# Kernel tuning notes

Hardware: AMD Instinct MI355X
Metric: run time of the kernel (lower is better)

The kernel has to match this reference:

```python
import jax, jax.numpy as jnp
import numpy as np
from jax import lax

# --- constants from init_kwargs ---
B, N = 1, 6
C_IN, MID, C_CTX, D = 512, 512, 80, 112
OGH, OGW = 256, 704
DSF = 16
FH, FW = OGH // DSF, OGW // DSF  # 16, 44
D_MIN, D_MAX = 2.0, 58.0
NX, NY, NZ = 128, 128, 1
VOXEL_SIZE = np.array([0.8, 0.8, 8.0], np.float32)
VOXEL_COORD = np.array([-51.2 + 0.4, -51.2 + 0.4, -5.0 + 4.0], np.float32)
VOXEL_NUM = np.array([NX, NY, NZ], np.int32)


def _conv(x, w, b=None):
    pad = (w.shape[-1] - 1) // 2
    y = lax.conv_general_dilated(x, w, (1, 1), [(pad, pad), (pad, pad)],
                                 dimension_numbers=('NCHW', 'OIHW', 'NCHW'))
    if b is not None:
        y = y + b[None, :, None, None]
    return y


def _depthnet(x, w_s1, w_s2, w_d1, w_d2, b_d, w_c1, w_c2, b_c):
    # BatchNorm layers at init (gamma=1, beta=0, running stats 0/1) are identity in eval
    x = jax.nn.relu(_conv(x, w_s1))
    x = jax.nn.relu(_conv(x, w_s2))
    depth_logits = _conv(jax.nn.relu(_conv(x, w_d1)), w_d2, b_d)   # [BN, D, FH, FW]
    context = _conv(jax.nn.relu(_conv(x, w_c1)), w_c2, b_c)        # [BN, C_CTX, FH, FW]
    return depth_logits, context


def _frustum():
    d = jnp.linspace(D_MIN, D_MAX, D, dtype=jnp.float32)            # [D]
    u = jnp.linspace(0.0, OGW - 1.0, FW, dtype=jnp.float32)         # [FW]
    v = jnp.linspace(0.0, OGH - 1.0, FH, dtype=jnp.float32)         # [FH]
    uu = jnp.broadcast_to(u[None, None, :], (D, FH, FW))
    vv = jnp.broadcast_to(v[None, :, None], (D, FH, FW))
    uv1 = jnp.stack([uu, vv, jnp.ones_like(uu)], axis=-1)           # [D,FH,FW,3]
    return uv1, d


def _geometry(sensor2ego, intrin, ida, bda):
    uv1, d = _frustum()
    ida_inv = jnp.linalg.inv(ida)                                   # [B,N,4,4]
    R_ida, t_ida = ida_inv[..., :3, :3], ida_inv[..., :3, 3]
    uv1_pre = jnp.einsum('bnij,dhwj->bndhwi', R_ida, uv1) + t_ida[:, :, None, None, None, :]
    K_inv = jnp.linalg.inv(intrin[..., :3, :3])
    rays = jnp.einsum('bnij,bndhwj->bndhwi', K_inv, uv1_pre)
    pts_cam = rays * d[None, None, :, None, None, None]             # [B,N,D,FH,FW,3]
    pts4 = jnp.concatenate([pts_cam, jnp.ones_like(pts_cam[..., :1])], axis=-1)
    pts_ego = jnp.einsum('bnij,bndhwj->bndhwi', sensor2ego, pts4)
    pts_ego = jnp.einsum('bij,bndhwj->bndhwi', bda, pts_ego)
    return pts_ego[..., :3]                                         # [B,N,D,FH,FW,3]


def _voxel_pooling(geom_xyz, feats):
    # geom_xyz: [B,N,D,FH,FW,3] int32 voxel coords; feats: [B,N,D,FH,FW,C]
    C = feats.shape[-1]
    g = geom_xyz.reshape(B, -1, 3)                                  # [B,M,3]
    valid = jnp.all((g >= 0) & (g < jnp.asarray(VOXEL_NUM)[None, None, :]), axis=-1)
    idx = g[..., 1] * NX + g[..., 0]                                # y*nx + x (z collapsed, NZ=1)
    idx = idx + jnp.arange(B, dtype=jnp.int32)[:, None] * (NY * NX)
    idx = jnp.where(valid, idx, B * NY * NX)                        # dump bucket
    f = feats.reshape(B * g.shape[1], C)
    out = jax.ops.segment_sum(f, idx.reshape(-1), num_segments=B * NY * NX + 1)
    out = out[:B * NY * NX].reshape(B, NY, NX, C)
    return jnp.transpose(out, (0, 3, 1, 2))                         # [B,C,NY,NX]


def setup_inputs() -> dict:
    key = jax.random.key(0)
    ks = jax.random.split(key, 8)

    def w(k, shape):
        fan_in = shape[1] * shape[2] * shape[3]
        return jax.random.normal(k, shape, jnp.float32) * np.sqrt(2.0 / fan_in)

    inp = {
        'source_features': jax.random.normal(ks[0], (B * N, C_IN, FH, FW), jnp.float32),
        'w_s1': w(ks[1], (MID, C_IN, 3, 3)),
        'w_s2': w(ks[2], (MID, MID, 3, 3)),
        'w_d1': w(ks[3], (MID, MID, 3, 3)),
        'w_d2': w(ks[4], (D, MID, 1, 1)),
        'b_d': jnp.zeros((D,), jnp.float32),
        'w_c1': w(ks[5], (MID, MID, 3, 3)),
        'w_c2': w(ks[6], (C_CTX, MID, 1, 1)),
        'b_c': jnp.zeros((C_CTX,), jnp.float32),
    }

    # realistic camera rig: 6 cameras yawed around ego, cam-forward (z) -> ego-forward
    base = np.array([[0., 0., 1.], [-1., 0., 0.], [0., -1., 0.]], np.float32)
    s2e = np.zeros((B, N, 4, 4), np.float32)
    for n in range(N):
        yaw = 2.0 * np.pi * n / N
        c, s = np.cos(yaw), np.sin(yaw)
        Rz = np.array([[c, -s, 0.], [s, c, 0.], [0., 0., 1.]], np.float32)
        s2e[0, n, :3, :3] = Rz @ base
        s2e[0, n, :3, 3] = [0.0, 0.0, 1.5]
        s2e[0, n, 3, 3] = 1.0
    intrin = np.zeros((B, N, 4, 4), np.float32)
    intrin[:, :] = np.eye(4, dtype=np.float32)
    intrin[:, :, 0, 0] = 560.0
    intrin[:, :, 1, 1] = 560.0
    intrin[:, :, 0, 2] = OGW / 2.0
    intrin[:, :, 1, 2] = OGH / 2.0
    ida = np.broadcast_to(np.eye(4, dtype=np.float32), (B, N, 4, 4)).copy()
    bda = np.broadcast_to(np.eye(4, dtype=np.float32), (B, 4, 4)).copy()

    inp['sensor2ego_mats'] = jnp.asarray(s2e)
    inp['intrin_mats'] = jnp.asarray(intrin)
    inp['ida_mats'] = jnp.asarray(ida)
    inp['bda_mat'] = jnp.asarray(bda)
    return inp


def reference(source_features, w_s1, w_s2, w_d1, w_d2, b_d, w_c1, w_c2, b_c,
              sensor2ego_mats, intrin_mats, ida_mats, bda_mat):
    depth_logits, context = _depthnet(source_features, w_s1, w_s2, w_d1, w_d2, b_d, w_c1, w_c2, b_c)
    depth_prob = jax.nn.softmax(depth_logits, axis=1)               # [BN,D,FH,FW]
    # depth-weighted context: [BN, C, D, FH, FW]
    feat = depth_prob[:, None, :, :, :] * context[:, :, None, :, :]
    feat = feat.reshape(B, N, C_CTX, D, FH, FW).transpose(0, 1, 3, 4, 5, 2)  # [B,N,D,FH,FW,C]
    pts_ego = _geometry(sensor2ego_mats, intrin_mats, ida_mats, bda_mat)
    vs = jnp.asarray(VOXEL_SIZE)
    vc = jnp.asarray(VOXEL_COORD)
    geom_xyz = ((pts_ego - (vc - vs / 2.0)) / vs).astype(jnp.int32)
    return _voxel_pooling(geom_xyz, feat)                            # [B,C,NY,NX]
```

## Files before the change

kernel.cpp:

```cpp
#include <hip/hip_runtime.h>


#define FH_ 16
#define FW_ 44
#define SP_ 704
#define XSTR 960
#define NIMG 6
#define CIN 512
#define DCH 112
#define CCTX 80
#define NXY 128
#define NVOX (NXY * NXY)
#define NPTS (NIMG * DCH * SP_)
#define CHUNK 64

#define NKC6 8
#define HCHK 360448
#define CIP 40

typedef unsigned short u16;
typedef unsigned int u32;
typedef __attribute__((ext_vector_type(8))) short bf16x8;
typedef __attribute__((ext_vector_type(4))) short s16x4;
typedef __attribute__((ext_vector_type(4))) float f32x4;
typedef __attribute__((ext_vector_type(16))) float f32x16;

__device__ __forceinline__ float bf2f(u16 b) {
    union { unsigned u; float f; } v; v.u = ((unsigned)b) << 16; return v.f;
}
__device__ __forceinline__ u16 f2bf(float f) {
    union { float f; unsigned u; } v; v.f = f;
    unsigned r = v.u + 0x7fffu + ((v.u >> 16) & 1u);
    return (u16)(r >> 16);
}
__device__ __forceinline__ int spad_of(int s) {
    return (s / 44) * 46 + (s % 44) + 47;
}
__device__ __forceinline__ void gld_lds16(const void* gsrc, void* ldst) {
    __builtin_amdgcn_global_load_lds(
        (const __attribute__((address_space(1))) u32*)gsrc,
        (__attribute__((address_space(3))) u32*)ldst, 16, 0, 0);
}
__device__ __forceinline__ _Float16* chunk6(_Float16* pA, _Float16* pB, int q, int n) {
    int c = q * 6 + n;
    return (c < 6) ? (pA + (size_t)c * HCHK) : (pB + (size_t)(c - 6) * HCHK);
}

__global__ void zero_k(float4* __restrict__ p, long n4) {
    long i = (long)blockIdx.x * blockDim.x + threadIdx.x;
    if (i < n4) p[i] = make_float4(0.f, 0.f, 0.f, 0.f);
}

__global__ void src_to_xt_k(const float* __restrict__ src, short* __restrict__ xt) {
    int e = blockIdx.x * 256 + threadIdx.x;
    if (e >= NIMG * SP_ * CIN) return;
    int ci = e & 511;
    int r = e >> 9;
    int s = r % SP_, n = r / SP_;
    float v = src[((size_t)n * CIN + ci) * SP_ + s];
    xt[(((size_t)n * 32 + (ci >> 4)) * XSTR + spad_of(s)) * 16 + (ci & 15)] = (short)f2bf(v);
}

__global__ void wsplit_k(const float* __restrict__ w, short* __restrict__ w2) {
    int e = blockIdx.x * 256 + threadIdx.x;
    if (e >= CIN * CIN) return;
    const int co = e >> 9, ci = e & 511;
    const float* wp = w + (size_t)e * 9;
#pragma unroll
    for (int t = 0; t < 9; ++t)
        w2[((((size_t)(ci >> 4) * 9) + t) * CIN + co) * 16 + (ci & 15)] = (short)f2bf(wp[t]);
}

__global__ void wsplit1_dual_k(const float* __restrict__ wd, short* __restrict__ od,
                               const float* __restrict__ wc, short* __restrict__ oc) {
    int i = blockIdx.x * 256 + threadIdx.x;
    if (i < DCH * CIN) od[i] = (short)f2bf(wd[i]);
    else if (i < DCH * CIN + CCTX * CIN) {
        int j = i - DCH * CIN;
        oc[j] = (short)f2bf(wc[j]);
    }
}

__global__ __launch_bounds__(256, 3) void conv6_k(
    const short* __restrict__ xt2, const short* __restrict__ w2,
    _Float16* __restrict__ pA, _Float16* __restrict__ pB)
{
    __shared__ short Xs[256 * 16];
    __shared__ short Wsh[1152 * 16];
    const int tid = threadIdx.x;
    const int lane = tid & 63, wave = tid >> 6;
    const int l31 = lane & 31, lh = lane >> 5;
    const int mw = wave >> 1, nw = wave & 1;

    const int bid = blockIdx.x;
    const int c16 = bid & 15;
    const int cb = c16 >> 2, q = c16 & 3;
    const int rest = bid >> 4;
    const int n = rest / 6, sb = rest - (rest / 6) * 6;

    const int s0 = sb * 128;
    const int co0 = cb * 128;
    const int base = spad_of(s0) - 47;

    const short* __restrict__ xq = xt2 + (((size_t)n * 32 + q * 8) * XSTR + base) * 16;
    const short* __restrict__ wq = w2 + (((size_t)(q * 8) * 9) * CIN + co0) * 16;

    int sloc[2];
#pragma unroll
    for (int mf = 0; mf < 2; ++mf)
        sloc[mf] = spad_of(s0 + mw * 64 + mf * 32 + l31) - base;

    const f32x16 z16 = {0.f,0.f,0.f,0.f,0.f,0.f,0.f,0.f,
                        0.f,0.f,0.f,0.f,0.f,0.f,0.f,0.f};
    f32x16 acc[2][2];
    acc[0][0] = z16; acc[0][1] = z16; acc[1][0] = z16; acc[1][1] = z16;

#define STAGE6(KC) do {                                                         \
    const short* xc = xq + (size_t)(KC) * (XSTR * 16) + lane * 8;               \
    const short* wc = wq + (size_t)(KC) * (9 * CIN * 16) + lane * 8;            \
    _Pragma("unroll")                                                           \
    for (int i = 0; i < 11; ++i) {                                              \
        const int sg = wave + 4 * i;                                            \
        if (sg < 8) {                                                           \
            gld_lds16(xc + sg * 512, &Xs[sg * 512]);                            \
        } else {                                                                \
            const int j = sg - 8, t = j >> 2, s4 = j & 3;                       \
            gld_lds16(wc + t * (CIN * 16) + s4 * 512, &Wsh[sg * 512 - 4096]);   \
        }                                                                       \
    }                                                                           \
} while (0)

    STAGE6(0);
    __syncthreads();

    constexpr int OFF[9] = {-47, -46, -45, -1, 0, 1, 45, 46, 47};
    for (int kc = 0; kc < NKC6; ++kc) {
#pragma unroll
        for (int t9 = 0; t9 < 9; ++t9) {
            const int off = OFF[t9];
            bf16x8 a0 = *(const bf16x8*)&Xs[(sloc[0] + off) * 16 + lh * 8];
            bf16x8 a1 = *(const bf16x8*)&Xs[(sloc[1] + off) * 16 + lh * 8];
            bf16x8 b0 = *(const bf16x8*)&Wsh[(t9 * 128 + nw * 64 + l31) * 16 + lh * 8];
            bf16x8 b1 = *(const bf16x8*)&Wsh[(t9 * 128 + nw * 64 + 32 + l31) * 16 + lh * 8];
            acc[0][0] = __builtin_amdgcn_mfma_f32_32x32x16_bf16(a0, b0, acc[0][0], 0, 0, 0);
            acc[0][1] = __builtin_amdgcn_mfma_f32_32x32x16_bf16(a0, b1, acc[0][1], 0, 0, 0);
            acc[1][0] = __builtin_amdgcn_mfma_f32_32x32x16_bf16(a1, b0, acc[1][0], 0, 0, 0);
            acc[1][1] = __builtin_amdgcn_mfma_f32_32x32x16_bf16(a1, b1, acc[1][1], 0, 0, 0);
        }
        __syncthreads();
        if (kc + 1 < NKC6) {
            STAGE6(kc + 1);
            __syncthreads();
        }
    }
#undef STAGE6

    _Float16* __restrict__ Pc = chunk6(pA, pB, q, n);
#pragma unroll
    for (int mf = 0; mf < 2; ++mf) {
        const int spb = mw * 64 + mf * 32 + 4 * lh;
#pragma unroll
        for (int r = 0; r < 16; ++r) {
            const int sg = s0 + spb + (r & 3) + 8 * (r >> 2);
            if (sg < SP_) {
                const size_t ro = (size_t)sg * 512 + co0 + nw * 64 + l31;
                Pc[ro] = (_Float16)acc[mf][0][r];
                Pc[ro + 32] = (_Float16)acc[mf][1][r];
            }
        }
    }
}

__global__ __launch_bounds__(256) void combine6_k(
    _Float16* __restrict__ pA, _Float16* __restrict__ pB, short* __restrict__ xout)
{
    const int i = blockIdx.x * 256 + threadIdx.x;
    if (i >= NIMG * SP_ * CIN / 4) return;
    const int e = i * 4;
    const int n = e / (SP_ * CIN);
    const int r = e - n * (SP_ * CIN);
    const int s = r >> 9, co = r & 511;
    union h4 { s16x4 s; _Float16 h[4]; };
    float v[4] = {0.f, 0.f, 0.f, 0.f};
#pragma unroll
    for (int q = 0; q < 4; ++q) {
        const _Float16* c = chunk6(pA, pB, q, n);
        h4 u; u.s = *(const s16x4*)(c + r);
#pragma unroll
        for (int j = 0; j < 4; ++j) v[j] += (float)u.h[j];
    }
    s16x4 o;
#pragma unroll
    for (int j = 0; j < 4; ++j) o[j] = (short)f2bf(fmaxf(v[j], 0.f));
    *(s16x4*)&xout[(((size_t)n * 32 + (co >> 4)) * XSTR + spad_of(s)) * 16 + (co & 15)] = o;
}

__global__ __launch_bounds__(256, 2) void gemm1x1d_k(
    const short* __restrict__ xA, const short* __restrict__ wA,
    const float* __restrict__ bA, float* __restrict__ oA,
    const short* __restrict__ xB, const short* __restrict__ wB,
    const float* __restrict__ bB, float* __restrict__ oB)
{
    const int sel = blockIdx.y;
    const short* __restrict__ xtin = sel ? xB : xA;
    const short* __restrict__ wb   = sel ? wB : wA;
    const float* __restrict__ bias = sel ? bB : bA;
    float* __restrict__ outT       = sel ? oB : oA;
    const int nst = sel ? (CCTX / 16) : (DCH / 16);
    const int nco = nst * 16;

    __shared__ short Wb[DCH * CIP];
    const int tid = threadIdx.x;
    const int s0 = blockIdx.x * 128, n = blockIdx.z;
    const int lane = tid & 63, wave = tid >> 6;
    const int kg = lane >> 4, lrow = lane & 15;
    const int swave = s0 + wave * 32;

    int arow[2];
#pragma unroll
    for (int ms = 0; ms < 2; ++ms)
        arow[ms] = spad_of(swave + ms * 16 + lrow);

    const f32x4 zero4 = {0.f, 0.f, 0.f, 0.f};
    f32x4 acc[2][7];
#pragma unroll
    for (int ms = 0; ms < 2; ++ms)
#pragma unroll
        for (int ns = 0; ns < 7; ++ns) acc[ms][ns] = zero4;

    const short* xb = xtin + (size_t)n * 32 * XSTR * 16;

    for (int kc = 0; kc < 16; ++kc) {
        __syncthreads();
#pragma unroll
        for (int it = 0; it < 2; ++it) {
            int q = it * 256 + tid;
            if (q < nco * 4) {
                int co = q >> 2, p = q & 3;
                *(bf16x8*)&Wb[co * CIP + p * 8] =
                    *(const bf16x8*)(wb + (size_t)co * CIN + kc * 32 + p * 8);
            }
        }
        __syncthreads();
        bf16x8 a[2];
#pragma unroll
        for (int ms = 0; ms < 2; ++ms) {
            const int kcc = 2 * kc + (kg >> 1);
            a[ms] = *(const bf16x8*)(xb + ((size_t)kcc * XSTR + arow[ms]) * 16 + (kg & 1) * 8);
        }
#pragma unroll
        for (int ns = 0; ns < 7; ++ns) {
            if (ns < nst) {
                int co = ns * 16 + lrow;
                bf16x8 b = *(const bf16x8*)&Wb[co * CIP + kg * 8];
#pragma unroll
                for (int ms = 0; ms < 2; ++ms)
                    acc[ms][ns] = __builtin_amdgcn_mfma_f32_16x16x32_bf16(
                        a[ms], b, acc[ms][ns], 0, 0, 0);
            }
        }
    }
#pragma unroll
    for (int ms = 0; ms < 2; ++ms)
#pragma unroll
        for (int ns = 0; ns < 7; ++ns) {
            if (ns < nst) {
#pragma unroll
                for (int r = 0; r < 4; ++r) {
                    int sg = swave + ms * 16 + kg * 4 + r;
                    if (sg < SP_) {
                        int co = ns * 16 + lrow;
                        outT[((size_t)n * SP_ + sg) * nco + co] = acc[ms][ns][r] + bias[co];
                    }
                }
            }
        }
}

__global__ __launch_bounds__(256) void softmax2_k(
    const float* __restrict__ lg, float* __restrict__ pr)
{
    const int p = blockIdx.x * 4 + (threadIdx.x >> 6);
    if (p >= NIMG * SP_) return;
    const int lane = threadIdx.x & 63;
    const float* lp = lg + (size_t)p * DCH;
    float v0 = lp[lane];
    float v1 = (lane < DCH - 64) ? lp[64 + lane] : -1e30f;
    float m = fmaxf(v0, v1);
#pragma unroll
    for (int o = 32; o; o >>= 1) m = fmaxf(m, __shfl_xor(m, o));
    float e0 = __expf(v0 - m);
    float e1 = (lane < DCH - 64) ? __expf(v1 - m) : 0.f;
    float s = e0 + e1;
#pragma unroll
    for (int o = 32; o; o >>= 1) s += __shfl_xor(s, o);
    const float inv = 1.f / s;
    float* pp = pr + (size_t)p * DCH;
    pp[lane] = e0 * inv;
    if (lane < DCH - 64) pp[64 + lane] = e1 * inv;
}

__device__ __forceinline__ void inv4(const double* M, double* inv) {
    inv[0]  =  M[5]*M[10]*M[15] - M[5]*M[11]*M[14] - M[9]*M[6]*M[15] + M[9]*M[7]*M[14] + M[13]*M[6]*M[11] - M[13]*M[7]*M[10];
    inv[4]  = -M[4]*M[10]*M[15] + M[4]*M[11]*M[14] + M[8]*M[6]*M[15] - M[8]*M[7]*M[14] - M[12]*M[6]*M[11] + M[12]*M[7]*M[10];
    inv[8]  =  M[4]*M[9]*M[15]  - M[4]*M[11]*M[13] - M[8]*M[5]*M[15] + M[8]*M[7]*M[13] + M[12]*M[5]*M[11] - M[12]*M[7]*M[9];
    inv[12] = -M[4]*M[9]*M[14]  + M[4]*M[10]*M[13] + M[8]*M[5]*M[14] - M[8]*M[6]*M[13] - M[12]*M[5]*M[10] + M[12]*M[6]*M[9];
    inv[1]  = -M[1]*M[10]*M[15] + M[1]*M[11]*M[14] + M[9]*M[2]*M[15] - M[9]*M[3]*M[14] - M[13]*M[2]*M[11] + M[13]*M[3]*M[10];
    inv[5]  =  M[0]*M[10]*M[15] - M[0]*M[11]*M[14] - M[8]*M[2]*M[15] + M[8]*M[3]*M[14] + M[12]*M[2]*M[11] - M[12]*M[3]*M[10];
    inv[9]  = -M[0]*M[9]*M[15]  + M[0]*M[11]*M[13] + M[8]*M[1]*M[15] - M[8]*M[3]*M[13] - M[12]*M[1]*M[11] + M[12]*M[3]*M[9];
    inv[13] =  M[0]*M[9]*M[14]  - M[0]*M[10]*M[13] - M[8]*M[1]*M[14] + M[8]*M[2]*M[13] + M[12]*M[1]*M[10] - M[12]*M[2]*M[9];
    inv[2]  =  M[1]*M[6]*M[15]  - M[1]*M[7]*M[14]  - M[5]*M[2]*M[15] + M[5]*M[3]*M[14] + M[13]*M[2]*M[7]  - M[13]*M[3]*M[6];
    inv[6]  = -M[0]*M[6]*M[15]  + M[0]*M[7]*M[14]  + M[4]*M[2]*M[15] - M[4]*M[3]*M[14] - M[12]*M[2]*M[7]  + M[12]*M[3]*M[6];
    inv[10] =  M[0]*M[5]*M[15]  - M[0]*M[7]*M[13]  - M[4]*M[1]*M[15] + M[4]*M[3]*M[13] + M[12]*M[1]*M[7]  - M[12]*M[3]*M[5];
    inv[14] = -M[0]*M[5]*M[14]  + M[0]*M[6]*M[13]  + M[4]*M[1]*M[14] - M[4]*M[2]*M[13] - M[12]*M[1]*M[6]  + M[12]*M[2]*M[5];
    inv[3]  = -M[1]*M[6]*M[11]  + M[1]*M[7]*M[10]  + M[5]*M[2]*M[11] - M[5]*M[3]*M[10] - M[9]*M[2]*M[7]   + M[9]*M[3]*M[6];
    inv[7]  =  M[0]*M[6]*M[11]  - M[0]*M[7]*M[10]  - M[4]*M[2]*M[11] + M[4]*M[3]*M[10] + M[8]*M[2]*M[7]   - M[8]*M[3]*M[6];
    inv[11] = -M[0]*M[5]*M[11]  + M[0]*M[7]*M[9]   + M[4]*M[1]*M[11] - M[4]*M[3]*M[9]  - M[8]*M[1]*M[7]   + M[8]*M[3]*M[5];
    inv[15] =  M[0]*M[5]*M[10]  - M[0]*M[6]*M[9]   - M[4]*M[1]*M[10] + M[4]*M[2]*M[9]  + M[8]*M[1]*M[6]   - M[8]*M[2]*M[5];
    double det = M[0]*inv[0] + M[1]*inv[4] + M[2]*inv[8] + M[3]*inv[12];
    double id = 1.0 / det;
#pragma unroll
    for (int i = 0; i < 16; ++i) inv[i] *= id;
}

__global__ void geom_setup_k(const float* __restrict__ s2e, const float* __restrict__ intrin,
                             const float* __restrict__ ida, const float* __restrict__ bda,
                             double* __restrict__ gc)
{
    const int n = threadIdx.x;
    if (n >= NIMG) return;
    double M[16], Iv[16];
#pragma unroll
    for (int i = 0; i < 16; ++i) M[i] = (double)ida[n * 16 + i];
    inv4(M, Iv);
    double R[3][3], tv[3];
#pragma unroll
    for (int r = 0; r < 3; ++r) {
#pragma unroll
        for (int c = 0; c < 3; ++c) R[r][c] = Iv[r * 4 + c];
        tv[r] = Iv[r * 4 + 3];
    }
    double K[3][3];
#pragma unroll
    for (int r = 0; r < 3; ++r)
#pragma unroll
        for (int c = 0; c < 3; ++c) K[r][c] = (double)intrin[n * 16 + r * 4 + c];
    double det = K[0][0] * (K[1][1] * K[2][2] - K[1][2] * K[2][1])
               - K[0][1] * (K[1][0] * K[2][2] - K[1][2] * K[2][0])
               + K[0][2] * (K[1][0] * K[2][1] - K[1][1] * K[2][0]);
    double id = 1.0 / det;
    double Ki[3][3];
    Ki[0][0] = (K[1][1] * K[2][2] - K[1][2] * K[2][1]) * id;
    Ki[0][1] = (K[0][2] * K[2][1] - K[0][1] * K[2][2]) * id;
    Ki[0][2] = (K[0][1] * K[1][2] - K[0][2] * K[1][1]) * id;
    Ki[1][0] = (K[1][2] * K[2][0] - K[1][0] * K[2][2]) * id;
    Ki[1][1] = (K[0][0] * K[2][2] - K[0][2] * K[2][0]) * id;
    Ki[1][2] = (K[0][2] * K[1][0] - K[0][0] * K[1][2]) * id;
    Ki[2][0] = (K[1][0] * K[2][1] - K[1][1] * K[2][0]) * id;
    Ki[2][1] = (K[0][1] * K[2][0] - K[0][0] * K[2][1]) * id;
    Ki[2][2] = (K[0][0] * K[1][1] - K[0][1] * K[1][0]) * id;
    double A[3][3], bv[3];
#pragma unroll
    for (int r = 0; r < 3; ++r) {
#pragma unroll
        for (int c = 0; c < 3; ++c)
            A[r][c] = Ki[r][0] * R[0][c] + Ki[r][1] * R[1][c] + Ki[r][2] * R[2][c];
        bv[r] = Ki[r][0] * tv[0] + Ki[r][1] * tv[1] + Ki[r][2] * tv[2];
    }
    double* g = gc + n * 24;
#pragma unroll
    for (int r = 0; r < 3; ++r)
#pragma unroll
        for (int c = 0; c < 3; ++c) g[r * 3 + c] = A[r][c];
#pragma unroll
    for (int r = 0; r < 3; ++r) g[9 + r] = bv[r];
#pragma unroll
    for (int r = 0; r < 3; ++r)
#pragma unroll
        for (int c = 0; c < 4; ++c) {
            double acc = 0.0;
#pragma unroll
            for (int k = 0; k < 4; ++k)
                acc += (double)bda[r * 4 + k] * (double)s2e[n * 16 + k * 4 + c];
            g[12 + r * 4 + c] = acc;
        }
}

__global__ __launch_bounds__(256) void point_voxel_k(
    const double* __restrict__ gc, int* __restrict__ vidx, int* __restrict__ cnt)
{
    const int i = blockIdx.x * 256 + threadIdx.x;
    if (i >= NPTS) return;
    const int lane = threadIdx.x & 63;
    const int n = i / (DCH * SP_);
    int r = i - n * (DCH * SP_);
    const int di = r / SP_;
    const int s = r - di * SP_;
    const int h = s / FW_, w = s - h * FW_;
    const double* g = gc + n * 24;
    const double u  = (double)(float)((double)w * (703.0 / 43.0));
    const double v  = (double)(float)((double)h * 17.0);
    const double dd = (double)(float)(2.0 + (double)di * (56.0 / 111.0));
    const double rx = g[0] * u + g[1] * v + g[2] + g[9];
    const double ry = g[3] * u + g[4] * v + g[5] + g[10];
    const double rz = g[6] * u + g[7] * v + g[8] + g[11];
    const double px = rx * dd, py = ry * dd, pz = rz * dd;
    const double ex = g[12] * px + g[13] * py + g[14] * pz + g[15];
    const double ey = g[16] * px + g[17] * py + g[18] * pz + g[19];
    const double ez = g[20] * px + g[21] * py + g[22] * pz + g[23];
    const double vs_xy = 0.8, vs_z = 8.0;
    const double offx = (double)(float)(-51.2 + 0.4) - vs_xy * 0.5;
    const double offz = (double)(float)(-5.0 + 4.0) - vs_z * 0.5;
    const int gx = (int)((ex - offx) / vs_xy);
    const int gy = (int)((ey - offx) / vs_xy);
    const int gz = (int)((ez - offz) / vs_z);
    const bool ok = (gx >= 0 && gx < NXY && gy >= 0 && gy < NXY && gz == 0);
    const int vv = ok ? (gy * NXY + gx) : -1;
    vidx[i] = vv;
    unsigned long long unresolved = __ballot(vv >= 0);
    while (unresolved) {
        const int src = __ffsll(unresolved) - 1;
        const int v0 = __shfl(vv, src);
        const unsigned long long grp = __ballot(vv == v0);
        if (lane == src) atomicAdd(&cnt[v0], __popcll(grp));
        unresolved &= ~grp;
    }
}

__global__ void prefix_k(const int* __restrict__ cnt, int* __restrict__ off,
                         int* __restrict__ cur) {
    __shared__ int part[256];
    const int t = threadIdx.x;
    int s = 0;
    for (int j = 0; j < 64; ++j) s += cnt[t * 64 + j];
    part[t] = s;
    __syncthreads();
    if (t == 0) {
        int run = 0;
        for (int k = 0; k < 256; ++k) { int v = part[k]; part[k] = run; run += v; }
    }
    __syncthreads();
    int base = part[t];
    for (int j = 0; j < 64; ++j) {
        off[t * 64 + j] = base;
        cur[t * 64 + j] = base;
        base += cnt[t * 64 + j];
    }
    if (t == 255) off[NVOX] = base;
}

__global__ __launch_bounds__(256) void fill_k(
    const int* __restrict__ vidx, const float* __restrict__ prob,
    int* __restrict__ cur, int2* __restrict__ pk) {
    int i = blockIdx.x * 256 + threadIdx.x;
    if (i >= NPTS) return;
    const int lane = threadIdx.x & 63;
    const int v = vidx[i];
    const int n = i / (DCH * SP_);
    int r = i - n * (DCH * SP_);
    const int di = r / SP_;
    const int s = r - di * SP_;
    float p = 0.f;
    if (v >= 0) p = prob[((size_t)n * SP_ + s) * DCH + di];

    int pos = -1;
    unsigned long long unresolved = __ballot(v >= 0);
    while (unresolved) {
        const int src = __ffsll(unresolved) - 1;
        const int v0 = __shfl(v, src);
        const unsigned long long grp = __ballot(v == v0);
        int base = 0;
        if (lane == src) base = atomicAdd(&cur[v0], __popcll(grp));
        base = __shfl(base, src);
        if (v == v0) {
            const int rank = __popcll(grp & ((1ull << lane) - 1ull));
            pos = base + rank;
        }
        unresolved &= ~grp;
    }
    if (v >= 0)
        pk[pos] = make_int2((v << 13) | (n * SP_ + s), __float_as_int(p));
}

__global__ __launch_bounds__(256) void gather2_k(
    const int2* __restrict__ pk, const int* __restrict__ off,
    const float* __restrict__ ctxT, float* __restrict__ accT)
{
    const int gtid = blockIdx.x * 256 + threadIdx.x;
    const int wid = gtid >> 6;
    const int lane = threadIdx.x & 63;
    const int total = off[NVOX];
    const int lo = wid * CHUNK;
    if (lo >= total) return;
    const int hi = min(lo + CHUNK, total);
    float a0 = 0.f, a1 = 0.f;
    int2 e = pk[lo];
    for (int k = lo; k < hi; ++k) {
        const int2 en = (k + 1 < hi) ? pk[k + 1] : make_int2(-1, 0);
        const float p = __int_as_float(e.y);
        const int ns = e.x & 8191;
        const float* cb = ctxT + (size_t)ns * CCTX;
        a0 = fmaf(p, cb[lane], a0);
        if (lane < CCTX - 64) a1 = fmaf(p, cb[64 + lane], a1);
        if ((en.x >> 13) != (e.x >> 13)) {
            float* ab = accT + (size_t)(e.x >> 13) * CCTX;
            atomicAdd(ab + lane, a0);
            if (lane < CCTX - 64) atomicAdd(ab + 64 + lane, a1);
            a0 = a1 = 0.f;
        }
        e = en;
    }
}

__global__ void transpose_out_k(const float* __restrict__ accT, float* __restrict__ out) {
    const int idx = blockIdx.x * 256 + threadIdx.x;
    if (idx >= CCTX * NVOX) return;
    const int c = idx >> 14;
    const int v = idx & 16383;
    out[idx] = accT[(size_t)v * CCTX + c];
}

#define O_WHIA  512
#define O_WHIB  1180160
#define O_XT0   2359808
#define O_XT1   3834368
#define O_XT2   5308928
#define O_WD2B  6783488
#define O_WC2B  6812160
#define O_DLG   6832640
#define O_DPR   7305728
#define O_CTX   7778816
#define O_PK    8116736
#define O_VIX   9062912
#define O_CNT   9536000
#define O_OFF   9552384
#define O_CUR   9568784
#define O_ACC   9585168

extern "C" void kernel_launch(void* const* d_in, const int* in_sizes, int n_in,
                              void* d_out, int out_size, void* d_ws, size_t ws_size,
                              hipStream_t stream)
{
    const float* src  = (const float*)d_in[0];
    const float* w_s1 = (const float*)d_in[1];
    const float* w_s2 = (const float*)d_in[2];
    const float* w_d1 = (const float*)d_in[3];
    const float* w_d2 = (const float*)d_in[4];
    const float* b_d  = (const float*)d_in[5];
    const float* w_c1 = (const float*)d_in[6];
    const float* w_c2 = (const float*)d_in[7];
    const float* b_c  = (const float*)d_in[8];
    const float* s2e  = (const float*)d_in[9];
    const float* intr = (const float*)d_in[10];
    const float* ida  = (const float*)d_in[11];
    const float* bda  = (const float*)d_in[12];

    double* gc = (double*)d_ws;
    float* ws   = (float*)d_ws;
    short* whiA = (short*)(ws + O_WHIA);
    _Float16* pA = (_Float16*)(ws + O_WHIB);
    _Float16* pB = (_Float16*)(ws + O_WD2B);
    short* xt0  = (short*)(ws + O_XT0);
    short* xt1  = (short*)(ws + O_XT1);
    short* xt2  = (short*)(ws + O_XT2);
    short* wd2b = (short*)(ws + O_WD2B);
    short* wc2b = (short*)(ws + O_WC2B);
    float* dlog = ws + O_DLG;
    float* dprb = ws + O_DPR;
    float* ctxT = ws + O_CTX;
    int2*  pk   = (int2*)(ws + O_PK);
    int* vidx   = (int*)(ws + O_VIX);
    int* cnt    = (int*)(ws + O_CNT);
    int* offs   = (int*)(ws + O_OFF);
    int* cur    = (int*)(ws + O_CUR);
    float* accT = ws + O_ACC;
    float* out  = (float*)d_out;

    const int CMB = (NIMG * SP_ * CIN / 4 + 255) / 256;

    zero_k<<<(2949120 / 4 + 255) / 256, 256, 0, stream>>>((float4*)xt0, 2949120 / 4);

    geom_setup_k<<<1, 64, 0, stream>>>(s2e, intr, ida, bda, gc);
    src_to_xt_k<<<(NIMG * SP_ * CIN + 255) / 256, 256, 0, stream>>>(src, xt0);

    wsplit_k<<<(CIN * CIN) / 256, 256, 0, stream>>>(w_s1, whiA);
    conv6_k<<<576, 256, 0, stream>>>(xt0, whiA, pA, pB);
    combine6_k<<<CMB, 256, 0, stream>>>(pA, pB, xt1);
    wsplit_k<<<(CIN * CIN) / 256, 256, 0, stream>>>(w_s2, whiA);
    conv6_k<<<576, 256, 0, stream>>>(xt1, whiA, pA, pB);
    combine6_k<<<CMB, 256, 0, stream>>>(pA, pB, xt0);
    wsplit_k<<<(CIN * CIN) / 256, 256, 0, stream>>>(w_c1, whiA);
    conv6_k<<<576, 256, 0, stream>>>(xt0, whiA, pA, pB);
    combine6_k<<<CMB, 256, 0, stream>>>(pA, pB, xt1);
    wsplit_k<<<(CIN * CIN) / 256, 256, 0, stream>>>(w_d1, whiA);
    conv6_k<<<576, 256, 0, stream>>>(xt0, whiA, pA, pB);
    combine6_k<<<CMB, 256, 0, stream>>>(pA, pB, xt2);

    wsplit1_dual_k<<<((DCH + CCTX) * CIN + 255) / 256, 256, 0, stream>>>(w_d2, wd2b, w_c2, wc2b);
    gemm1x1d_k<<<dim3(6, 2, NIMG), 256, 0, stream>>>(xt2, wd2b, b_d, dlog,
                                                     xt1, wc2b, b_c, ctxT);
    softmax2_k<<<(NIMG * SP_ + 3) / 4, 256, 0, stream>>>(dlog, dprb);

    zero_k<<<(NVOX / 4 + 255) / 256, 256, 0, stream>>>((float4*)cnt, NVOX / 4);
    point_voxel_k<<<(NPTS + 255) / 256, 256, 0, stream>>>(gc, vidx, cnt);
    prefix_k<<<1, 256, 0, stream>>>(cnt, offs, cur);
    fill_k<<<(NPTS + 255) / 256, 256, 0, stream>>>(vidx, dprb, cur, pk);

    zero_k<<<(1310720 / 4 + 255) / 256, 256, 0, stream>>>((float4*)accT, 1310720 / 4);
    {
        const int waves = (NPTS + CHUNK - 1) / CHUNK;
        const int blocks = (waves + 3) / 4;
        gather2_k<<<blocks, 256, 0, stream>>>(pk, offs, ctxT, accT);
    }
    transpose_out_k<<<(CCTX * NVOX + 255) / 256, 256, 0, stream>>>(accT, out);

    (void)in_sizes; (void)n_in; (void)out_size; (void)ws_size;
}
```

Measured before the change: 391.6 us.

## Double-buffer conv LDS staging with smaller blocks and batch weight splits

The 3x3 conv kernel now uses 128-thread blocks that each cover 64 output channels, twice as many blocks. LDS for the input and weight tiles is double-buffered, so the next K-chunk is prefetched while MFMAs run on the current one, leaving one barrier per iteration instead of two. Weight reformatting for two convs is fused into one launch, with the second layer's weights placed in the otherwise unused xt2 buffer. The trade-off is that each input tile is now staged by twice as many blocks, which raises global and LDS traffic for activations.

Result: slower. 421.4 us (+7.6%).

```diff
diff --git a/kernel.cpp b/kernel.cpp
--- a/kernel.cpp
+++ b/kernel.cpp
@@ -14,7 +14,7 @@
 #define NPTS (NIMG * DCH * SP_)
 #define CHUNK 64
 
-#define NKC6 8
+#define NKC7 8
 #define HCHK 360448
 #define CIP 40
 
@@ -61,14 +61,18 @@
     xt[(((size_t)n * 32 + (ci >> 4)) * XSTR + spad_of(s)) * 16 + (ci & 15)] = (short)f2bf(v);
 }
 
-__global__ void wsplit_k(const float* __restrict__ w, short* __restrict__ w2) {
-    int e = blockIdx.x * 256 + threadIdx.x;
-    if (e >= CIN * CIN) return;
+__global__ void wsplit2_k(const float* __restrict__ wA, short* __restrict__ oA,
+                          const float* __restrict__ wB, short* __restrict__ oB) {
+    int i = blockIdx.x * 256 + threadIdx.x;
+    if (i >= 2 * CIN * CIN) return;
+    const int e = i & (CIN * CIN - 1);
+    const float* __restrict__ w = (i < CIN * CIN) ? wA : wB;
+    short* __restrict__ o = (i < CIN * CIN) ? oA : oB;
     const int co = e >> 9, ci = e & 511;
     const float* wp = w + (size_t)e * 9;
 #pragma unroll
     for (int t = 0; t < 9; ++t)
-        w2[((((size_t)(ci >> 4) * 9) + t) * CIN + co) * 16 + (ci & 15)] = (short)f2bf(wp[t]);
+        o[((((size_t)(ci >> 4) * 9) + t) * CIN + co) * 16 + (ci & 15)] = (short)f2bf(wp[t]);
 }
 
 __global__ void wsplit1_dual_k(const float* __restrict__ wd, short* __restrict__ od,
@@ -81,25 +85,24 @@
     }
 }
 
-__global__ __launch_bounds__(256, 3) void conv6_k(
+__global__ __launch_bounds__(128, 2) void conv7_k(
     const short* __restrict__ xt2, const short* __restrict__ w2,
     _Float16* __restrict__ pA, _Float16* __restrict__ pB)
 {
-    __shared__ short Xs[256 * 16];
-    __shared__ short Wsh[1152 * 16];
+    __shared__ short Xs[2][256 * 16];
+    __shared__ short Wsh[2][576 * 16];
     const int tid = threadIdx.x;
     const int lane = tid & 63, wave = tid >> 6;
     const int l31 = lane & 31, lh = lane >> 5;
-    const int mw = wave >> 1, nw = wave & 1;
 
     const int bid = blockIdx.x;
-    const int c16 = bid & 15;
-    const int cb = c16 >> 2, q = c16 & 3;
-    const int rest = bid >> 4;
+    const int c32 = bid & 31;
+    const int cb = c32 >> 2, q = c32 & 3;
+    const int rest = bid >> 5;
     const int n = rest / 6, sb = rest - (rest / 6) * 6;
 
     const int s0 = sb * 128;
-    const int co0 = cb * 128;
+    const int co0 = cb * 64;
     const int base = spad_of(s0) - 47;
 
     const short* __restrict__ xq = xt2 + (((size_t)n * 32 + q * 8) * XSTR + base) * 16;
@@ -108,62 +111,62 @@
     int sloc[2];
 #pragma unroll
     for (int mf = 0; mf < 2; ++mf)
-        sloc[mf] = spad_of(s0 + mw * 64 + mf * 32 + l31) - base;
+        sloc[mf] = spad_of(s0 + wave * 64 + mf * 32 + l31) - base;
 
     const f32x16 z16 = {0.f,0.f,0.f,0.f,0.f,0.f,0.f,0.f,
                         0.f,0.f,0.f,0.f,0.f,0.f,0.f,0.f};
     f32x16 acc[2][2];
     acc[0][0] = z16; acc[0][1] = z16; acc[1][0] = z16; acc[1][1] = z16;
 
-#define STAGE6(KC) do {                                                         \
+#define STAGE7(BUF, KC) do {                                                    \
     const short* xc = xq + (size_t)(KC) * (XSTR * 16) + lane * 8;               \
     const short* wc = wq + (size_t)(KC) * (9 * CIN * 16) + lane * 8;            \
     _Pragma("unroll")                                                           \
-    for (int i = 0; i < 11; ++i) {                                              \
-        const int sg = wave + 4 * i;                                            \
+    for (int i = 0; i < 13; ++i) {                                              \
+        const int sg = wave + 2 * i;                                            \
         if (sg < 8) {                                                           \
-            gld_lds16(xc + sg * 512, &Xs[sg * 512]);                            \
+            gld_lds16(xc + sg * 512, &Xs[BUF][sg * 512]);                       \
         } else {                                                                \
-            const int j = sg - 8, t = j >> 2, s4 = j & 3;                       \
-            gld_lds16(wc + t * (CIN * 16) + s4 * 512, &Wsh[sg * 512 - 4096]);   \
+            const int j = sg - 8;                                               \
+            gld_lds16(wc + (j >> 1) * (CIN * 16) + (j & 1) * 512,               \
+                      &Wsh[BUF][j * 512]);                                      \
         }                                                                       \
     }                                                                           \
 } while (0)
 
-    STAGE6(0);
+    STAGE7(0, 0);
     __syncthreads();
 
     constexpr int OFF[9] = {-47, -46, -45, -1, 0, 1, 45, 46, 47};
-    for (int kc = 0; kc < NKC6; ++kc) {
+    for (int kc = 0; kc < NKC7; ++kc) {
+        if (kc + 1 < NKC7) STAGE7((kc + 1) & 1, kc + 1);
+        const short* __restrict__ Xb = Xs[kc & 1];
+        const short* __restrict__ Wb = Wsh[kc & 1];
 #pragma unroll
         for (int t9 = 0; t9 < 9; ++t9) {
             const int off = OFF[t9];
-            bf16x8 a0 = *(const bf16x8*)&Xs[(sloc[0] + off) * 16 + lh * 8];
-            bf16x8 a1 = *(const bf16x8*)&Xs[(sloc[1] + off) * 16 + lh * 8];
-            bf16x8 b0 = *(const bf16x8*)&Wsh[(t9 * 128 + nw * 64 + l31) * 16 + lh * 8];
-            bf16x8 b1 = *(const bf16x8*)&Wsh[(t9 * 128 + nw * 64 + 32 + l31) * 16 + lh * 8];
+            bf16x8 a0 = *(const bf16x8*)&Xb[(sloc[0] + off) * 16 + lh * 8];
+            bf16x8 a1 = *(const bf16x8*)&Xb[(sloc[1] + off) * 16 + lh * 8];
+            bf16x8 b0 = *(const bf16x8*)&Wb[(t9 * 64 + l31) * 16 + lh * 8];
+            bf16x8 b1 = *(const bf16x8*)&Wb[(t9 * 64 + 32 + l31) * 16 + lh * 8];
             acc[0][0] = __builtin_amdgcn_mfma_f32_32x32x16_bf16(a0, b0, acc[0][0], 0, 0, 0);
             acc[0][1] = __builtin_amdgcn_mfma_f32_32x32x16_bf16(a0, b1, acc[0][1], 0, 0, 0);
             acc[1][0] = __builtin_amdgcn_mfma_f32_32x32x16_bf16(a1, b0, acc[1][0], 0, 0, 0);
             acc[1][1] = __builtin_amdgcn_mfma_f32_32x32x16_bf16(a1, b1, acc[1][1], 0, 0, 0);
         }
         __syncthreads();
-        if (kc + 1 < NKC6) {
-            STAGE6(kc + 1);
-            __syncthreads();
-        }
-    }
-#undef STAGE6
+    }
+#undef STAGE7
 
     _Float16* __restrict__ Pc = chunk6(pA, pB, q, n);
 #pragma unroll
     for (int mf = 0; mf < 2; ++mf) {
-        const int spb = mw * 64 + mf * 32 + 4 * lh;
+        const int spb = wave * 64 + mf * 32 + 4 * lh;
 #pragma unroll
         for (int r = 0; r < 16; ++r) {
             const int sg = s0 + spb + (r & 3) + 8 * (r >> 2);
             if (sg < SP_) {
-                const size_t ro = (size_t)sg * 512 + co0 + nw * 64 + l31;
+                const size_t ro = (size_t)sg * 512 + co0 + l31;
                 Pc[ro] = (_Float16)acc[mf][0][r];
                 Pc[ro + 32] = (_Float16)acc[mf][1][r];
             }
@@ -558,6 +561,7 @@
     double* gc = (double*)d_ws;
     float* ws   = (float*)d_ws;
     short* whiA = (short*)(ws + O_WHIA);
+    short* whiC = (short*)(ws + O_XT2);
     _Float16* pA = (_Float16*)(ws + O_WHIB);
     _Float16* pB = (_Float16*)(ws + O_WD2B);
     short* xt0  = (short*)(ws + O_XT0);
@@ -583,17 +587,15 @@
     geom_setup_k<<<1, 64, 0, stream>>>(s2e, intr, ida, bda, gc);
     src_to_xt_k<<<(NIMG * SP_ * CIN + 255) / 256, 256, 0, stream>>>(src, xt0);
 
-    wsplit_k<<<(CIN * CIN) / 256, 256, 0, stream>>>(w_s1, whiA);
-    conv6_k<<<576, 256, 0, stream>>>(xt0, whiA, pA, pB);
+    wsplit2_k<<<(2 * CIN * CIN) / 256, 256, 0, stream>>>(w_s1, whiA, w_s2, whiC);
+    conv7_k<<<1152, 128, 0, stream>>>(xt0, whiA, pA, pB);
     combine6_k<<<CMB, 256, 0, stream>>>(pA, pB, xt1);
-    wsplit_k<<<(CIN * CIN) / 256, 256, 0, stream>>>(w_s2, whiA);
-    conv6_k<<<576, 256, 0, stream>>>(xt1, whiA, pA, pB);
+    conv7_k<<<1152, 128, 0, stream>>>(xt1, whiC, pA, pB);
     combine6_k<<<CMB, 256, 0, stream>>>(pA, pB, xt0);
-    wsplit_k<<<(CIN * CIN) / 256, 256, 0, stream>>>(w_c1, whiA);
-    conv6_k<<<576, 256, 0, stream>>>(xt0, whiA, pA, pB);
+    wsplit2_k<<<(2 * CIN * CIN) / 256, 256, 0, stream>>>(w_c1, whiA, w_d1, whiC);
+    conv7_k<<<1152, 128, 0, stream>>>(xt0, whiA, pA, pB);
     combine6_k<<<CMB, 256, 0, stream>>>(pA, pB, xt1);
-    wsplit_k<<<(CIN * CIN) / 256, 256, 0, stream>>>(w_d1, whiA);
-    conv6_k<<<576, 256, 0, stream>>>(xt0, whiA, pA, pB);
+    conv7_k<<<1152, 128, 0, stream>>>(xt0, whiC, pA, pB);
     combine6_k<<<CMB, 256, 0, stream>>>(pA, pB, xt2);
 
     wsplit1_dual_k<<<((DCH + CCTX) * CIN + 255) / 256, 256, 0, stream>>>(w_d2, wd2b, w_c2, wc2b);
```

## Fuse context and depth 3x3 convs into one launch and batch weight prep

Applied to the files above, without the earlier changes.

The context and depth branch 3x3 convolutions share the same input, so they now run in one kernel launch. Each block picks a layer and splits K into two halves, where the old kernel split it into four, and a dual combine kernel reduces both layers at once. Weight conversion for two conv layers is done per launch, with the second layer's weights written into the xt2 buffer before it is reused. The 1x1 GEMM now uses 64-row tiles to launch more blocks. This cuts launch count and gives larger grids, but the fused conv does longer K loops per block and depends on careful buffer aliasing.

After: 371.2 us. 5.2% less time.

```diff
diff --git a/kernel.cpp b/kernel.cpp
--- a/kernel.cpp
+++ b/kernel.cpp
@@ -41,8 +41,7 @@
         (const __attribute__((address_space(1))) u32*)gsrc,
         (__attribute__((address_space(3))) u32*)ldst, 16, 0, 0);
 }
-__device__ __forceinline__ _Float16* chunk6(_Float16* pA, _Float16* pB, int q, int n) {
-    int c = q * 6 + n;
+__device__ __forceinline__ _Float16* chunkc(_Float16* pA, _Float16* pB, int c) {
     return (c < 6) ? (pA + (size_t)c * HCHK) : (pB + (size_t)(c - 6) * HCHK);
 }
 
@@ -61,14 +60,18 @@
     xt[(((size_t)n * 32 + (ci >> 4)) * XSTR + spad_of(s)) * 16 + (ci & 15)] = (short)f2bf(v);
 }
 
-__global__ void wsplit_k(const float* __restrict__ w, short* __restrict__ w2) {
-    int e = blockIdx.x * 256 + threadIdx.x;
-    if (e >= CIN * CIN) return;
+__global__ void wsplit2_k(const float* __restrict__ wA, short* __restrict__ oA,
+                          const float* __restrict__ wB, short* __restrict__ oB) {
+    int i = blockIdx.x * 256 + threadIdx.x;
+    if (i >= 2 * CIN * CIN) return;
+    const int e = i & (CIN * CIN - 1);
+    const float* __restrict__ w = (i < CIN * CIN) ? wA : wB;
+    short* __restrict__ o = (i < CIN * CIN) ? oA : oB;
     const int co = e >> 9, ci = e & 511;
     const float* wp = w + (size_t)e * 9;
 #pragma unroll
     for (int t = 0; t < 9; ++t)
-        w2[((((size_t)(ci >> 4) * 9) + t) * CIN + co) * 16 + (ci & 15)] = (short)f2bf(wp[t]);
+        o[((((size_t)(ci >> 4) * 9) + t) * CIN + co) * 16 + (ci & 15)] = (short)f2bf(wp[t]);
 }
 
 __global__ void wsplit1_dual_k(const float* __restrict__ wd, short* __restrict__ od,
@@ -155,7 +158,100 @@
     }
 #undef STAGE6
 
-    _Float16* __restrict__ Pc = chunk6(pA, pB, q, n);
+    _Float16* __restrict__ Pc = chunkc(pA, pB, q * 6 + n);
+#pragma unroll
+    for (int mf = 0; mf < 2; ++mf) {
+        const int spb = mw * 64 + mf * 32 + 4 * lh;
+#pragma unroll
+        for (int r = 0; r < 16; ++r) {
+            const int sg = s0 + spb + (r & 3) + 8 * (r >> 2);
+            if (sg < SP_) {
+                const size_t ro = (size_t)sg * 512 + co0 + nw * 64 + l31;
+                Pc[ro] = (_Float16)acc[mf][0][r];
+                Pc[ro + 32] = (_Float16)acc[mf][1][r];
+            }
+        }
+    }
+}
+
+__global__ __launch_bounds__(256, 3) void conv6d_k(
+    const short* __restrict__ xt2, const short* __restrict__ wA,
+    const short* __restrict__ wB,
+    _Float16* __restrict__ pA, _Float16* __restrict__ pB)
+{
+    __shared__ short Xs[256 * 16];
+    __shared__ short Wsh[1152 * 16];
+    const int tid = threadIdx.x;
+    const int lane = tid & 63, wave = tid >> 6;
+    const int l31 = lane & 31, lh = lane >> 5;
+    const int mw = wave >> 1, nw = wave & 1;
+
+    const int bid = blockIdx.x;
+    const int c16 = bid & 15;
+    const int cb = c16 >> 2;
+    const int layer = (c16 >> 1) & 1, q = c16 & 1;
+    const int rest = bid >> 4;
+    const int n = rest / 6, sb = rest - (rest / 6) * 6;
+
+    const int s0 = sb * 128;
+    const int co0 = cb * 128;
+    const int base = spad_of(s0) - 47;
+
+    const short* __restrict__ w2 = layer ? wB : wA;
+    const short* __restrict__ xq = xt2 + (((size_t)n * 32 + q * 16) * XSTR + base) * 16;
+    const short* __restrict__ wq = w2 + (((size_t)(q * 16) * 9) * CIN + co0) * 16;
+
+    int sloc[2];
+#pragma unroll
+    for (int mf = 0; mf < 2; ++mf)
+        sloc[mf] = spad_of(s0 + mw * 64 + mf * 32 + l31) - base;
+
+    const f32x16 z16 = {0.f,0.f,0.f,0.f,0.f,0.f,0.f,0.f,
+                        0.f,0.f,0.f,0.f,0.f,0.f,0.f,0.f};
+    f32x16 acc[2][2];
+    acc[0][0] = z16; acc[0][1] = z16; acc[1][0] = z16; acc[1][1] = z16;
+
+#define STAGE6D(KC) do {                                                        \
+    const short* xc = xq + (size_t)(KC) * (XSTR * 16) + lane * 8;               \
+    const short* wc = wq + (size_t)(KC) * (9 * CIN * 16) + lane * 8;            \
+    _Pragma("unroll")                                                           \
+    for (int i = 0; i < 11; ++i) {                                              \
+        const int sg = wave + 4 * i;                                            \
+        if (sg < 8) {                                                           \
+            gld_lds16(xc + sg * 512, &Xs[sg * 512]);                            \
+        } else {                                                                \
+            const int j = sg - 8, t = j >> 2, s4 = j & 3;                       \
+            gld_lds16(wc + t * (CIN * 16) + s4 * 512, &Wsh[sg * 512 - 4096]);   \
+        }                                                                       \
+    }                                                                           \
+} while (0)
+
+    STAGE6D(0);
+    __syncthreads();
+
+    constexpr int OFF[9] = {-47, -46, -45, -1, 0, 1, 45, 46, 47};
+    for (int kc = 0; kc < 16; ++kc) {
+#pragma unroll
+        for (int t9 = 0; t9 < 9; ++t9) {
+            const int off = OFF[t9];
+            bf16x8 a0 = *(const bf16x8*)&Xs[(sloc[0] + off) * 16 + lh * 8];
+            bf16x8 a1 = *(const bf16x8*)&Xs[(sloc[1] + off) * 16 + lh * 8];
+            bf16x8 b0 = *(const bf16x8*)&Wsh[(t9 * 128 + nw * 64 + l31) * 16 + lh * 8];
+            bf16x8 b1 = *(const bf16x8*)&Wsh[(t9 * 128 + nw * 64 + 32 + l31) * 16 + lh * 8];
+            acc[0][0] = __builtin_amdgcn_mfma_f32_32x32x16_bf16(a0, b0, acc[0][0], 0, 0, 0);
+            acc[0][1] = __builtin_amdgcn_mfma_f32_32x32x16_bf16(a0, b1, acc[0][1], 0, 0, 0);
+            acc[1][0] = __builtin_amdgcn_mfma_f32_32x32x16_bf16(a1, b0, acc[1][0], 0, 0, 0);
+            acc[1][1] = __builtin_amdgcn_mfma_f32_32x32x16_bf16(a1, b1, acc[1][1], 0, 0, 0);
+        }
+        __syncthreads();
+        if (kc + 1 < 16) {
+            STAGE6D(kc + 1);
+            __syncthreads();
+        }
+    }
+#undef STAGE6D
+
+    _Float16* __restrict__ Pc = chunkc(pA, pB, layer * 12 + q * 6 + n);
 #pragma unroll
     for (int mf = 0; mf < 2; ++mf) {
         const int spb = mw * 64 + mf * 32 + 4 * lh;
@@ -184,7 +280,7 @@
     float v[4] = {0.f, 0.f, 0.f, 0.f};
 #pragma unroll
     for (int q = 0; q < 4; ++q) {
-        const _Float16* c = chunk6(pA, pB, q, n);
+        const _Float16* c = chunkc(pA, pB, q * 6 + n);
         h4 u; u.s = *(const s16x4*)(c + r);
 #pragma unroll
         for (int j = 0; j < 4; ++j) v[j] += (float)u.h[j];
@@ -192,6 +288,34 @@
     s16x4 o;
 #pragma unroll
     for (int j = 0; j < 4; ++j) o[j] = (short)f2bf(fmaxf(v[j], 0.f));
+    *(s16x4*)&xout[(((size_t)n * 32 + (co >> 4)) * XSTR + spad_of(s)) * 16 + (co & 15)] = o;
+}
+
+__global__ __launch_bounds__(256) void combine6d_k(
+    _Float16* __restrict__ pA, _Float16* __restrict__ pB,
+    short* __restrict__ o0, short* __restrict__ o1)
+{
+    const int i = blockIdx.x * 256 + threadIdx.x;
+    if (i >= 2 * NIMG * SP_ * CIN / 4) return;
+    const int L = i / (NIMG * SP_ * CIN / 4);
+    const int j0 = i - L * (NIMG * SP_ * CIN / 4);
+    const int e = j0 * 4;
+    const int n = e / (SP_ * CIN);
+    const int r = e - n * (SP_ * CIN);
+    const int s = r >> 9, co = r & 511;
+    union h4 { s16x4 s; _Float16 h[4]; };
+    float v[4] = {0.f, 0.f, 0.f, 0.f};
+#pragma unroll
+    for (int q = 0; q < 2; ++q) {
+        const _Float16* c = chunkc(pA, pB, L * 12 + q * 6 + n);
+        h4 u; u.s = *(const s16x4*)(c + r);
+#pragma unroll
+        for (int j = 0; j < 4; ++j) v[j] += (float)u.h[j];
+    }
+    s16x4 o;
+#pragma unroll
+    for (int j = 0; j < 4; ++j) o[j] = (short)f2bf(fmaxf(v[j], 0.f));
+    short* __restrict__ xout = L ? o1 : o0;
     *(s16x4*)&xout[(((size_t)n * 32 + (co >> 4)) * XSTR + spad_of(s)) * 16 + (co & 15)] = o;
 }
 
@@ -211,22 +335,17 @@
 
     __shared__ short Wb[DCH * CIP];
     const int tid = threadIdx.x;
-    const int s0 = blockIdx.x * 128, n = blockIdx.z;
+    const int s0 = blockIdx.x * 64, n = blockIdx.z;
     const int lane = tid & 63, wave = tid >> 6;
     const int kg = lane >> 4, lrow = lane & 15;
-    const int swave = s0 + wave * 32;
-
-    int arow[2];
-#pragma unroll
-    for (int ms = 0; ms < 2; ++ms)
-        arow[ms] = spad_of(swave + ms * 16 + lrow);
+    const int swave = s0 + wave * 16;
+
+    const int arow = spad_of(swave + lrow);
 
     const f32x4 zero4 = {0.f, 0.f, 0.f, 0.f};
-    f32x4 acc[2][7];
-#pragma unroll
-    for (int ms = 0; ms < 2; ++ms)
-#pragma unroll
-        for (int ns = 0; ns < 7; ++ns) acc[ms][ns] = zero4;
+    f32x4 acc[7];
+#pragma unroll
+    for (int ns = 0; ns < 7; ++ns) acc[ns] = zero4;
 
     const short* xb = xtin + (size_t)n * 32 * XSTR * 16;
 
@@ -242,39 +361,28 @@
             }
         }
         __syncthreads();
-        bf16x8 a[2];
-#pragma unroll
-        for (int ms = 0; ms < 2; ++ms) {
-            const int kcc = 2 * kc + (kg >> 1);
-            a[ms] = *(const bf16x8*)(xb + ((size_t)kcc * XSTR + arow[ms]) * 16 + (kg & 1) * 8);
-        }
+        const int kcc = 2 * kc + (kg >> 1);
+        bf16x8 a = *(const bf16x8*)(xb + ((size_t)kcc * XSTR + arow) * 16 + (kg & 1) * 8);
 #pragma unroll
         for (int ns = 0; ns < 7; ++ns) {
             if (ns < nst) {
                 int co = ns * 16 + lrow;
                 bf16x8 b = *(const bf16x8*)&Wb[co * CIP + kg * 8];
-#pragma unroll
-                for (int ms = 0; ms < 2; ++ms)
-                    acc[ms][ns] = __builtin_amdgcn_mfma_f32_16x16x32_bf16(
-                        a[ms], b, acc[ms][ns], 0, 0, 0);
+                acc[ns] = __builtin_amdgcn_mfma_f32_16x16x32_bf16(a, b, acc[ns], 0, 0, 0);
             }
         }
     }
 #pragma unroll
-    for (int ms = 0; ms < 2; ++ms)
-#pragma unroll
-        for (int ns = 0; ns < 7; ++ns) {
-            if (ns < nst) {
-#pragma unroll
-                for (int r = 0; r < 4; ++r) {
-                    int sg = swave + ms * 16 + kg * 4 + r;
-                    if (sg < SP_) {
-                        int co = ns * 16 + lrow;
-                        outT[((size_t)n * SP_ + sg) * nco + co] = acc[ms][ns][r] + bias[co];
-                    }
-                }
+    for (int ns = 0; ns < 7; ++ns) {
+        if (ns < nst) {
+#pragma unroll
+            for (int r = 0; r < 4; ++r) {
+                const int sg = swave + kg * 4 + r;
+                const int co = ns * 16 + lrow;
+                outT[((size_t)n * SP_ + sg) * nco + co] = acc[ns][r] + bias[co];
             }
         }
+    }
 }
 
 __global__ __launch_bounds__(256) void softmax2_k(
@@ -558,6 +666,7 @@
     double* gc = (double*)d_ws;
     float* ws   = (float*)d_ws;
     short* whiA = (short*)(ws + O_WHIA);
+    short* whiC = (short*)(ws + O_XT2);
     _Float16* pA = (_Float16*)(ws + O_WHIB);
     _Float16* pB = (_Float16*)(ws + O_WD2B);
     short* xt0  = (short*)(ws + O_XT0);
@@ -583,22 +692,18 @@
     geom_setup_k<<<1, 64, 0, stream>>>(s2e, intr, ida, bda, gc);
     src_to_xt_k<<<(NIMG * SP_ * CIN + 255) / 256, 256, 0, stream>>>(src, xt0);
 
-    wsplit_k<<<(CIN * CIN) / 256, 256, 0, stream>>>(w_s1, whiA);
+    wsplit2_k<<<(2 * CIN * CIN) / 256, 256, 0, stream>>>(w_s1, whiA, w_s2, whiC);
     conv6_k<<<576, 256, 0, stream>>>(xt0, whiA, pA, pB);
     combine6_k<<<CMB, 256, 0, stream>>>(pA, pB, xt1);
-    wsplit_k<<<(CIN * CIN) / 256, 256, 0, stream>>>(w_s2, whiA);
-    conv6_k<<<576, 256, 0, stream>>>(xt1, whiA, pA, pB);
+    conv6_k<<<576, 256, 0, stream>>>(xt1, whiC, pA, pB);
     combine6_k<<<CMB, 256, 0, stream>>>(pA, pB, xt0);
-    wsplit_k<<<(CIN * CIN) / 256, 256, 0, stream>>>(w_c1, whiA);
-    conv6_k<<<576, 256, 0, stream>>>(xt0, whiA, pA, pB);
-    combine6_k<<<CMB, 256, 0, stream>>>(pA, pB, xt1);
-    wsplit_k<<<(CIN * CIN) / 256, 256, 0, stream>>>(w_d1, whiA);
-    conv6_k<<<576, 256, 0, stream>>>(xt0, whiA, pA, pB);
-    combine6_k<<<CMB, 256, 0, stream>>>(pA, pB, xt2);
+    wsplit2_k<<<(2 * CIN * CIN) / 256, 256, 0, stream>>>(w_c1, whiA, w_d1, whiC);
+    conv6d_k<<<576, 256, 0, stream>>>(xt0, whiA, whiC, pA, pB);
+    combine6d_k<<<2 * CMB, 256, 0, stream>>>(pA, pB, xt1, xt2);
 
     wsplit1_dual_k<<<((DCH + CCTX) * CIN + 255) / 256, 256, 0, stream>>>(w_d2, wd2b, w_c2, wc2b);
-    gemm1x1d_k<<<dim3(6, 2, NIMG), 256, 0, stream>>>(xt2, wd2b, b_d, dlog,
-                                                     xt1, wc2b, b_c, ctxT);
+    gemm1x1d_k<<<dim3(11, 2, NIMG), 256, 0, stream>>>(xt2, wd2b, b_d, dlog,
+                                                      xt1, wc2b, b_c, ctxT);
     softmax2_k<<<(NIMG * SP_ + 3) / 4, 256, 0, stream>>>(dlog, dprb);
 
     zero_k<<<(NVOX / 4 + 255) / 256, 256, 0, stream>>>((float4*)cnt, NVOX / 4);
```
